# Kernel tuning notes

Hardware: AMD Instinct MI355X
Metric: run time of the kernel (lower is better)

The kernel has to match this reference:

```python
import jax, jax.numpy as jnp
import numpy as np

DIM = 768
H = 12          # num query heads
KV = 6          # num kv heads
GS = H // KV    # group size = 2
HD = DIM // H   # head dim = 64


def setup_inputs() -> dict:
    key = jax.random.key(0)
    ks = jax.random.split(key, 6)
    B, P = 8, 1024
    s = DIM ** -0.5
    x = jax.random.normal(ks[0], (B, P, DIM), dtype=jnp.float32)
    Wq = jax.random.normal(ks[1], (DIM, DIM), dtype=jnp.float32) * s
    Wk = jax.random.normal(ks[2], (DIM, KV * HD), dtype=jnp.float32) * s
    Wv = jax.random.normal(ks[3], (DIM, KV * HD), dtype=jnp.float32) * s
    Wp = jax.random.normal(ks[4], (DIM, DIM), dtype=jnp.float32) * s
    bp = jnp.zeros((DIM,), dtype=jnp.float32)
    return {"x": x, "Wq": Wq, "Wk": Wk, "Wv": Wv, "Wp": Wp, "bp": bp}


def reference(x, Wq, Wk, Wv, Wp, bp):
    B, P, C = x.shape
    scale = HD ** -0.5
    # projections; consecutive heads i*GS..(i+1)*GS-1 form kv-group i (torch.split dim=1)
    q = (x @ Wq).reshape(B, P, KV, GS, HD).transpose(0, 2, 3, 1, 4) * scale  # [B,KV,GS,P,d]
    k = (x @ Wk).reshape(B, P, KV, HD).transpose(0, 2, 1, 3)                 # [B,KV,P,d]
    v = (x @ Wv).reshape(B, P, KV, HD).transpose(0, 2, 1, 3)                 # [B,KV,P,d]

    scores = jnp.einsum('bghqd,bgkd->bghqk', q, k)      # [B,KV,GS,P,P]
    w = jax.nn.softmax(scores, axis=-1)                  # attn_drop=0 (eval)
    att = jnp.einsum('bghqk,bgkd->bghqd', w, v)          # [B,KV,GS,P,d]

    # per-group row-matched gaussian-ish noise (torch get_gaussian), vectorized over KV groups
    y = P * HD
    flat = att.reshape(B, KV, GS, y)                     # rows = groups within kv-group
    M = jax.random.uniform(jax.random.key(42), (KV, GS, y), dtype=flat.dtype)
    di = jnp.arange(min(GS, y))
    M = M.at[:, di, di].set(0.0)                         # sparse: zero diagonal
    m_mean = M.mean(axis=-1, keepdims=True)
    m_std = jnp.std(M, axis=-1, ddof=1, keepdims=True)   # torch.std is unbiased
    m_std = jnp.where(m_std == 0, jnp.ones_like(m_std), m_std)
    Z = (M - m_mean) / m_std                             # [KV,GS,y], shared across batch
    r_mean = flat.mean(axis=-1, keepdims=True)           # [B,KV,GS,1]
    r_std = jnp.std(flat, axis=-1, ddof=1, keepdims=True)
    flat = flat - (Z[None] * r_std + r_mean)

    att = flat.reshape(B, KV, GS, P, HD).reshape(B, H, P, HD)
    out = att.transpose(0, 2, 1, 3).reshape(B, P, C) @ Wp + bp  # proj_drop=0
    return out
```

## Files before the change

### kernel.cpp

```cpp
#include <hip/hip_runtime.h>
#include <hip/hip_bf16.h>
#include <math.h>


#define NTHREADS 256

typedef __bf16 bf16x8 __attribute__((ext_vector_type(8)));
typedef float f32x4 __attribute__((ext_vector_type(4)));

#define MFMA16(a, b, c) __builtin_amdgcn_mfma_f32_16x16x32_bf16(a, b, c, 0, 0, 0)

#define QSCALE 0.18033688011112042f

__device__ __forceinline__ float fexp2(float x) {
#if __has_builtin(__builtin_amdgcn_exp2f)
    return __builtin_amdgcn_exp2f(x);
#else
    return __expf(x * 0.6931471805599453f);
#endif
}

__device__ __forceinline__ void gload16(const void* g, void* l) {
    __builtin_amdgcn_global_load_lds(
        (const __attribute__((address_space(1))) void*)g,
        (__attribute__((address_space(3))) void*)l, 16, 0, 0);
}

__device__ __forceinline__ unsigned rotl_u32(unsigned x, int r) {
    return (x << r) | (x >> (32 - r));
}
__device__ __forceinline__ void threefry_0_42(unsigned x0, unsigned x1,
                                              unsigned& o0, unsigned& o1) {
    const unsigned ks0 = 0u, ks1 = 42u, ks2 = 0u ^ 42u ^ 0x1BD11BDAu;
    x0 += ks0; x1 += ks1;
#define R4(a,b,c,d) \
    x0 += x1; x1 = rotl_u32(x1,a); x1 ^= x0; \
    x0 += x1; x1 = rotl_u32(x1,b); x1 ^= x0; \
    x0 += x1; x1 = rotl_u32(x1,c); x1 ^= x0; \
    x0 += x1; x1 = rotl_u32(x1,d); x1 ^= x0;
    R4(13,15,26,6)   x0 += ks1; x1 += ks2 + 1u;
    R4(17,29,16,24)  x0 += ks2; x1 += ks0 + 2u;
    R4(13,15,26,6)   x0 += ks0; x1 += ks1 + 3u;
    R4(17,29,16,24)  x0 += ks1; x1 += ks2 + 4u;
    R4(13,15,26,6)   x0 += ks2; x1 += ks0 + 5u;
#undef R4
    o0 = x0; o1 = x1;
}
__device__ __forceinline__ float tf_uniform(unsigned i) {
    unsigned o0, o1;
    threefry_0_42(0u, i, o0, o1);
    unsigned bits = o0 ^ o1;
    return __uint_as_float((bits >> 9) | 0x3f800000u) - 1.0f;
}

__device__ __forceinline__ float wave_sum64(float v) {
#pragma unroll
    for (int off = 32; off; off >>= 1) v += __shfl_xor(v, off, 64);
    return v;
}

__device__ __forceinline__ unsigned short bf16_rne(float x) {
    unsigned u = __float_as_uint(x);
    return (unsigned short)((u + 0x7fffu + ((u >> 16) & 1u)) >> 16);
}
__device__ __forceinline__ unsigned pack_bf16x2(float lo, float hi) {
    return (unsigned)bf16_rne(lo) | ((unsigned)bf16_rne(hi) << 16);
}
__device__ __forceinline__ float bfu(unsigned v) {
    return __uint_as_float(v << 16);
}

__global__ __launch_bounds__(NTHREADS) void prep_k(
    const float* __restrict__ x, const float* __restrict__ Wq,
    const float* __restrict__ Wk, const float* __restrict__ Wv,
    const float* __restrict__ Wp,
    unsigned short* __restrict__ xb, unsigned short* __restrict__ wqt,
    unsigned short* __restrict__ wkt, unsigned short* __restrict__ wvt,
    unsigned short* __restrict__ wpt,
    unsigned short* __restrict__ zb, float* __restrict__ zpart)
{
    __shared__ float rbuf[8];
    int blk = blockIdx.x;
    if (blk < 1536) {
#pragma unroll
        for (int j = 0; j < 4; ++j) {
            int i = blk * 1024 + j * 256 + threadIdx.x;
            float4 v = ((const float4*)x)[i];
            uint2 u;
            u.x = pack_bf16x2(v.x, v.y);
            u.y = pack_bf16x2(v.z, v.w);
            *(uint2*)(xb + (size_t)i * 4) = u;
        }
    } else if (blk < 1920) {
        int zc = blk - 1536;
        int row = zc >> 5, chunk = zc & 31;
        int g = row & 1;
        int j0 = chunk * 2048;
        float sum = 0.f, sumsq = 0.f;
        for (int t = threadIdx.x; t < 2048; t += NTHREADS) {
            int j = j0 + t;
            unsigned i = (unsigned)row * 65536u + (unsigned)j;
            float m = tf_uniform(i);
            if (j == g) m = 0.f;
            zb[i] = bf16_rne(m);
            sum += m; sumsq += m * m;
        }
        sum = wave_sum64(sum); sumsq = wave_sum64(sumsq);
        int lane = threadIdx.x & 63, wv = threadIdx.x >> 6;
        if (lane == 0) { rbuf[wv] = sum; rbuf[4 + wv] = sumsq; }
        __syncthreads();
        if (threadIdx.x == 0) {
            zpart[zc * 2]     = rbuf[0] + rbuf[1] + rbuf[2] + rbuf[3];
            zpart[zc * 2 + 1] = rbuf[4] + rbuf[5] + rbuf[6] + rbuf[7];
        }
    } else {
        int id = blk - 1920;
        const float* W; unsigned short* Wt; int N;
        if (id < 144)      { W = Wq; Wt = wqt; N = 768; }
        else if (id < 216) { W = Wk; Wt = wkt; N = 384; id -= 144; }
        else if (id < 288) { W = Wv; Wt = wvt; N = 384; id -= 216; }
        else               { W = Wp; Wt = wpt; N = 768; id -= 288; }
        int ntn = N >> 6;
        int kt = id / ntn, nt = id % ntn;
        int k0 = kt * 64, n0 = nt * 64;
        int t = threadIdx.x;
        int tn = t & 63, tk = t >> 6;
        float r[16];
#pragma unroll
        for (int j = 0; j < 16; ++j)
            r[j] = W[(size_t)(k0 + tk * 16 + j) * N + n0 + tn];
        uint4 u0, u1;
        u0.x = pack_bf16x2(r[0], r[1]);   u0.y = pack_bf16x2(r[2], r[3]);
        u0.z = pack_bf16x2(r[4], r[5]);   u0.w = pack_bf16x2(r[6], r[7]);
        u1.x = pack_bf16x2(r[8], r[9]);   u1.y = pack_bf16x2(r[10], r[11]);
        u1.z = pack_bf16x2(r[12], r[13]); u1.w = pack_bf16x2(r[14], r[15]);
        unsigned short* dst = Wt + (size_t)(n0 + tn) * 768 + k0 + tk * 16;
        *(uint4*)dst = u0;
        *(uint4*)(dst + 8) = u1;
    }
}

__device__ __forceinline__ void mfma_tile_compute(
    const unsigned short* __restrict__ A, const unsigned short* __restrict__ Bt,
    int row0, int col0,
    unsigned short* As, unsigned short* Bs, f32x4 acc[4][4])
{
    const int tid = threadIdx.x;
    const int w = tid >> 6, lane = tid & 63;
    const int c = lane & 15, g = lane >> 4;
    const int m0 = (w & 1) * 64, n0 = (w >> 1) * 64;

#pragma unroll
    for (int mi = 0; mi < 4; ++mi)
#pragma unroll
        for (int ni = 0; ni < 4; ++ni) acc[mi][ni] = (f32x4){0.f, 0.f, 0.f, 0.f};

    const unsigned short* Ag0 = A + (size_t)(row0 + w * 16 + c) * 768 + g * 8;
    const unsigned short* Ag1 = A + (size_t)(row0 + (w + 4) * 16 + c) * 768 + g * 8;
    const unsigned short* Bg0 = Bt + (size_t)(col0 + w * 16 + c) * 768 + g * 8;
    const unsigned short* Bg1 = Bt + (size_t)(col0 + (w + 4) * 16 + c) * 768 + g * 8;
    unsigned short* Al0 = As + w * 1024 + lane * 8;
    unsigned short* Al1 = As + (w + 4) * 1024 + lane * 8;
    unsigned short* Bl0 = Bs + w * 1024 + lane * 8;
    unsigned short* Bl1 = Bs + (w + 4) * 1024 + lane * 8;

    for (int k0 = 0; k0 < 768; k0 += 64) {
        __syncthreads();
        gload16(Ag0 + k0,      Al0);
        gload16(Ag0 + k0 + 32, Al0 + 512);
        gload16(Ag1 + k0,      Al1);
        gload16(Ag1 + k0 + 32, Al1 + 512);
        gload16(Bg0 + k0,      Bl0);
        gload16(Bg0 + k0 + 32, Bl0 + 512);
        gload16(Bg1 + k0,      Bl1);
        gload16(Bg1 + k0 + 32, Bl1 + 512);
        __syncthreads();
#pragma unroll
        for (int ks = 0; ks < 2; ++ks) {
            bf16x8 aA[4], bB[4];
#pragma unroll
            for (int mi = 0; mi < 4; ++mi)
                aA[mi] = *(const bf16x8*)&As[(size_t)((m0 >> 4) + mi) * 1024 + ks * 512 + g * 128 + c * 8];
#pragma unroll
            for (int ni = 0; ni < 4; ++ni)
                bB[ni] = *(const bf16x8*)&Bs[(size_t)((n0 >> 4) + ni) * 1024 + ks * 512 + g * 128 + c * 8];
#pragma unroll
            for (int mi = 0; mi < 4; ++mi)
#pragma unroll
                for (int ni = 0; ni < 4; ++ni)
                    acc[mi][ni] = MFMA16(aA[mi], bB[ni], acc[mi][ni]);
        }
    }
}

__global__ __launch_bounds__(NTHREADS) void qkv_mfma_k(
    const unsigned short* __restrict__ xb, const unsigned short* __restrict__ wqt,
    const unsigned short* __restrict__ wkt, const unsigned short* __restrict__ wvt,
    unsigned short* __restrict__ qbh, unsigned short* __restrict__ kb2,
    unsigned short* __restrict__ vb2)
{
    __shared__ unsigned short As[8192];
    __shared__ unsigned short Bs[8192];
    int nb = blockIdx.x;
    int y0 = blockIdx.y * 128;
    f32x4 acc[4][4];

    const int tid = threadIdx.x;
    const int w = tid >> 6, lane = tid & 63;
    const int c = lane & 15, g = lane >> 4;
    const int m0 = (w & 1) * 64, n0 = (w >> 1) * 64;

    if (nb < 9) {
        int row0 = (nb < 6) ? nb * 128 : (nb - 6) * 128;
        const unsigned short* Wt = (nb < 6) ? wqt : wkt;
        mfma_tile_compute(Wt, xb, row0, y0, As, Bs, acc);
        float scale = (nb < 6) ? QSCALE : 1.0f;
#pragma unroll
        for (int mi = 0; mi < 4; ++mi) {
            int ocol = row0 + m0 + mi * 16 + g * 4;
#pragma unroll
            for (int ni = 0; ni < 4; ++ni) {
                int pglob = y0 + n0 + ni * 16 + c;
                int b = pglob >> 10, pin = pglob & 1023;
                ushort4 u;
                u.x = bf16_rne(acc[mi][ni][0] * scale);
                u.y = bf16_rne(acc[mi][ni][1] * scale);
                u.z = bf16_rne(acc[mi][ni][2] * scale);
                u.w = bf16_rne(acc[mi][ni][3] * scale);
                if (nb < 6) {
                    int h = ocol >> 6, d0 = ocol & 63;
                    *(ushort4*)&qbh[(((size_t)b * 12 + h) * 1024 + pin) * 64 + d0] = u;
                } else {
                    int kv = ocol >> 6, d0 = ocol & 63;
                    int kt = pin >> 7, key = pin & 127;
                    *(ushort4*)&kb2[((((size_t)(b * 6 + kv) * 8 + kt) * 8 + (d0 >> 3)) * 128
                                     + key) * 8 + (d0 & 7)] = u;
                }
            }
        }
    } else {
        int col0 = (nb - 9) * 128;
        mfma_tile_compute(xb, wvt, y0, col0, As, Bs, acc);
#pragma unroll
        for (int mi = 0; mi < 4; ++mi) {
            int pglob = y0 + m0 + mi * 16 + g * 4;
            int b = pglob >> 10, pin = pglob & 1023;
            int kt = pin >> 7, pg = (pin & 127) >> 3, p8 = pin & 7;
#pragma unroll
            for (int ni = 0; ni < 4; ++ni) {
                int vcol = col0 + n0 + ni * 16 + c;
                int kv = vcol >> 6, d = vcol & 63;
                ushort4 u;
                u.x = bf16_rne(acc[mi][ni][0]);
                u.y = bf16_rne(acc[mi][ni][1]);
                u.z = bf16_rne(acc[mi][ni][2]);
                u.w = bf16_rne(acc[mi][ni][3]);
                *(ushort4*)&vb2[((((size_t)(b * 6 + kv) * 8 + kt) * 16 + pg) * 64 + d) * 8 + p8] = u;
            }
        }
    }
}

__global__ __launch_bounds__(NTHREADS) void proj_mfma_k(
    const unsigned short* __restrict__ attb, const unsigned short* __restrict__ wpt,
    const float* __restrict__ bp, float* __restrict__ out)
{
    __shared__ unsigned short As[8192];
    __shared__ unsigned short Bs[8192];
    int row0 = blockIdx.x * 128, col0 = blockIdx.y * 128;
    f32x4 acc[4][4];
    mfma_tile_compute(wpt, attb, row0, col0, As, Bs, acc);

    const int tid = threadIdx.x;
    const int w = tid >> 6, lane = tid & 63;
    const int c = lane & 15, g = lane >> 4;
    const int m0 = (w & 1) * 64, n0 = (w >> 1) * 64;
#pragma unroll
    for (int mi = 0; mi < 4; ++mi) {
        int ocol = row0 + m0 + mi * 16 + g * 4;
        float4 bias = *(const float4*)&bp[ocol];
#pragma unroll
        for (int ni = 0; ni < 4; ++ni) {
            int p = col0 + n0 + ni * 16 + c;
            float4 u;
            u.x = acc[mi][ni][0] + bias.x;
            u.y = acc[mi][ni][1] + bias.y;
            u.z = acc[mi][ni][2] + bias.z;
            u.w = acc[mi][ni][3] + bias.w;
            *(float4*)&out[(size_t)p * 768 + ocol] = u;
        }
    }
}

#define LDP 136
__global__ __launch_bounds__(NTHREADS) void attn_mfma_k(
    const unsigned short* __restrict__ qbh, const unsigned short* __restrict__ kb2,
    const unsigned short* __restrict__ vb2, unsigned short* __restrict__ attb,
    float* __restrict__ spart)
{
    __shared__ unsigned short P_lds[4 * 32 * LDP];
    __shared__ float l_s[4][32];
    __shared__ float sbuf[8];

    const int qt0 = blockIdx.x * 128;
    const int h = blockIdx.y, b = blockIdx.z, kv = h >> 1;
    const int tid = threadIdx.x;
    const int w = tid >> 6, lane = tid & 63;
    const int c = lane & 15, g = lane >> 4;

    const unsigned short* qh = qbh + (((size_t)b * 12 + h) * 1024 + qt0 + w * 32) * 64;
    const unsigned short* kbase = kb2 + ((size_t)(b * 6 + kv) * 8) * 8192;
    const unsigned short* vbase = vb2 + ((size_t)(b * 6 + kv) * 8) * 8192;
    unsigned short* Pw = P_lds + w * 32 * LDP;

    bf16x8 bQ[2][2];
#pragma unroll
    for (int ks = 0; ks < 2; ++ks) {
        bQ[ks][0] = *(const bf16x8*)(qh + (size_t)(c) * 64 + ks * 32 + g * 8);
        bQ[ks][1] = *(const bf16x8*)(qh + (size_t)(16 + c) * 64 + ks * 32 + g * 8);
    }

    f32x4 O[2][4];
#pragma unroll
    for (int i = 0; i < 2; ++i)
#pragma unroll
        for (int j = 0; j < 4; ++j) O[i][j] = (f32x4){0.f, 0.f, 0.f, 0.f};
    float l_r[2] = {0.f, 0.f};

    for (int t = 0; t < 8; ++t) {
        const unsigned short* kt = kbase + (size_t)t * 8192;
        const unsigned short* vt = vbase + (size_t)t * 8192;

        bf16x8 aK[2][8];
#pragma unroll
        for (int ks = 0; ks < 2; ++ks)
#pragma unroll
            for (int mb = 0; mb < 8; ++mb)
                aK[ks][mb] = *(const bf16x8*)(kt + ((size_t)(ks * 4 + g) * 128 + mb * 16 + c) * 8);

        f32x4 S[8][2];
#pragma unroll
        for (int mb = 0; mb < 8; ++mb) {
            S[mb][0] = (f32x4){0.f, 0.f, 0.f, 0.f};
            S[mb][1] = (f32x4){0.f, 0.f, 0.f, 0.f};
        }
#pragma unroll
        for (int ks = 0; ks < 2; ++ks)
#pragma unroll
            for (int mb = 0; mb < 8; ++mb) {
                S[mb][0] = MFMA16(aK[ks][mb], bQ[ks][0], S[mb][0]);
                S[mb][1] = MFMA16(aK[ks][mb], bQ[ks][1], S[mb][1]);
            }

        bf16x8 bV[4][4];
#pragma unroll
        for (int ks = 0; ks < 4; ++ks)
#pragma unroll
            for (int nb = 0; nb < 4; ++nb)
                bV[ks][nb] = *(const bf16x8*)(vt + ((size_t)(ks * 4 + g) * 64 + nb * 16 + c) * 8);

#pragma unroll
        for (int qn = 0; qn < 2; ++qn) {
            float lt = 0.f;
#pragma unroll
            for (int mb = 0; mb < 8; ++mb) {
                float p0 = fexp2(S[mb][qn][0]);
                float p1 = fexp2(S[mb][qn][1]);
                float p2 = fexp2(S[mb][qn][2]);
                float p3 = fexp2(S[mb][qn][3]);
                lt += (p0 + p1) + (p2 + p3);
                uint2 uu;
                uu.x = pack_bf16x2(p0, p1);
                uu.y = pack_bf16x2(p2, p3);
                *(uint2*)&Pw[(size_t)(qn * 16 + c) * LDP + mb * 16 + g * 4] = uu;
            }
            lt += __shfl_xor(lt, 16, 64);
            lt += __shfl_xor(lt, 32, 64);
            l_r[qn] += lt;
        }

#pragma unroll
        for (int ks = 0; ks < 4; ++ks) {
            bf16x8 aP0 = *(const bf16x8*)&Pw[(size_t)(c) * LDP + ks * 32 + g * 8];
            bf16x8 aP1 = *(const bf16x8*)&Pw[(size_t)(16 + c) * LDP + ks * 32 + g * 8];
#pragma unroll
            for (int nb = 0; nb < 4; ++nb) {
                O[0][nb] = MFMA16(aP0, bV[ks][nb], O[0][nb]);
                O[1][nb] = MFMA16(aP1, bV[ks][nb], O[1][nb]);
            }
        }
    }
    if (g == 0) { l_s[w][c] = l_r[0]; l_s[w][16 + c] = l_r[1]; }
    f32x4 li0 = *(f32x4*)&l_s[w][g * 4];
    f32x4 li1 = *(f32x4*)&l_s[w][16 + g * 4];
    float inv0[4], inv1[4];
#pragma unroll
    for (int r = 0; r < 4; ++r) { inv0[r] = 1.f / li0[r]; inv1[r] = 1.f / li1[r]; }
    unsigned short* ob = attb + ((size_t)b * 1024 + qt0 + w * 32) * 768 + h * 64;
    float psum = 0.f, psumsq = 0.f;
#pragma unroll
    for (int r = 0; r < 4; ++r) {
#pragma unroll
        for (int nb = 0; nb < 4; ++nb) {
            float o0 = O[0][nb][r] * inv0[r];
            float o1 = O[1][nb][r] * inv1[r];
            psum += o0 + o1;
            psumsq += o0 * o0 + o1 * o1;
            ob[(size_t)(g * 4 + r) * 768 + nb * 16 + c]      = bf16_rne(o0);
            ob[(size_t)(16 + g * 4 + r) * 768 + nb * 16 + c] = bf16_rne(o1);
        }
    }
    psum = wave_sum64(psum); psumsq = wave_sum64(psumsq);
    if (lane == 0) { sbuf[w] = psum; sbuf[4 + w] = psumsq; }
    __syncthreads();
    if (tid == 0) {
        int idx = ((b * 12 + h) * 8 + blockIdx.x) * 2;
        spart[idx]     = sbuf[0] + sbuf[1] + sbuf[2] + sbuf[3];
        spart[idx + 1] = sbuf[4] + sbuf[5] + sbuf[6] + sbuf[7];
    }
}

__global__ __launch_bounds__(NTHREADS) void stats2_k(
    unsigned short* __restrict__ attb, const unsigned short* __restrict__ zb,
    const float* __restrict__ spart, const float* __restrict__ zpart)
{
    int blk = blockIdx.x;
    int bh = blk >> 3, ch = blk & 7;
    int b = bh / 12, h = bh % 12;
    float zs = 0.f, zs2 = 0.f, rs = 0.f, rs2 = 0.f;
#pragma unroll
    for (int cc = 0; cc < 32; ++cc) {
        zs  += zpart[(h * 32 + cc) * 2];
        zs2 += zpart[(h * 32 + cc) * 2 + 1];
    }
#pragma unroll
    for (int cc = 0; cc < 8; ++cc) {
        rs  += spart[(bh * 8 + cc) * 2];
        rs2 += spart[(bh * 8 + cc) * 2 + 1];
    }
    float m_mean = zs * (1.f / 65536.f);
    float m_var  = (zs2 - 65536.f * m_mean * m_mean) * (1.f / 65535.f);
    float m_sd   = sqrtf(fmaxf(m_var, 0.f));
    if (m_sd == 0.f) m_sd = 1.f;
    float r_mean = rs * (1.f / 65536.f);
    float r_var  = (rs2 - 65536.f * r_mean * r_mean) * (1.f / 65535.f);
    float r_sd   = sqrtf(fmaxf(r_var, 0.f));
    float a = r_sd / m_sd;
    float bc = m_mean * a - r_mean;

    unsigned short* base = attb + ((size_t)b * 1024 + ch * 128) * 768 + h * 64;
    const unsigned short* zrow = zb + (size_t)h * 65536 + (size_t)ch * 8192;
    for (int f = threadIdx.x; f < 1024; f += NTHREADS) {
        int p = f >> 3, dq = (f & 7) * 8;
        unsigned short* ptr = base + (size_t)p * 768 + dq;
        uint4 u = *(const uint4*)ptr;
        uint4 zu = *(const uint4*)(zrow + (size_t)f * 8);
        float v0 = bfu(u.x)       - bfu(zu.x)       * a + bc;
        float v1 = bfu(u.x >> 16) - bfu(zu.x >> 16) * a + bc;
        float v2 = bfu(u.y)       - bfu(zu.y)       * a + bc;
        float v3 = bfu(u.y >> 16) - bfu(zu.y >> 16) * a + bc;
        float v4 = bfu(u.z)       - bfu(zu.z)       * a + bc;
        float v5 = bfu(u.z >> 16) - bfu(zu.z >> 16) * a + bc;
        float v6 = bfu(u.w)       - bfu(zu.w)       * a + bc;
        float v7 = bfu(u.w >> 16) - bfu(zu.w >> 16) * a + bc;
        uint4 o;
        o.x = pack_bf16x2(v0, v1);
        o.y = pack_bf16x2(v2, v3);
        o.z = pack_bf16x2(v4, v5);
        o.w = pack_bf16x2(v6, v7);
        *(uint4*)ptr = o;
    }
}

extern "C" void kernel_launch(void* const* d_in, const int* in_sizes, int n_in,
                              void* d_out, int out_size, void* d_ws, size_t ws_size,
                              hipStream_t stream) {
    const float* x  = (const float*)d_in[0];
    const float* Wq = (const float*)d_in[1];
    const float* Wk = (const float*)d_in[2];
    const float* Wv = (const float*)d_in[3];
    const float* Wp = (const float*)d_in[4];
    const float* bp = (const float*)d_in[5];
    float* out = (float*)d_out;

    float* ws    = (float*)d_ws;
    float* zpart = ws;
    float* spart = zpart + 768;
    unsigned short* zb   = (unsigned short*)(spart + 1536);
    unsigned short* xb   = zb + 786432;
    unsigned short* wqt  = xb + 6291456;
    unsigned short* wkt  = wqt + 589824;
    unsigned short* wvt  = wkt + 294912;
    unsigned short* wpt  = wvt + 294912;
    unsigned short* qbh  = wpt + 589824;
    unsigned short* kb2  = qbh + 6291456;
    unsigned short* vb2  = kb2 + 3145728;
    unsigned short* attb = vb2 + 3145728;

    prep_k<<<2352, NTHREADS, 0, stream>>>(x, Wq, Wk, Wv, Wp,
                                          xb, wqt, wkt, wvt, wpt, zb, zpart);
    qkv_mfma_k<<<dim3(12, 64), NTHREADS, 0, stream>>>(xb, wqt, wkt, wvt, qbh, kb2, vb2);
    attn_mfma_k<<<dim3(8, 12, 8), NTHREADS, 0, stream>>>(qbh, kb2, vb2, attb, spart);
    stats2_k<<<768, NTHREADS, 0, stream>>>(attb, zb, spart, zpart);
    proj_mfma_k<<<dim3(6, 64), NTHREADS, 0, stream>>>(attb, wpt, bp, out);
}
```

Before: 222.4 us.

## Double-buffer LDS tiles in MFMA GEMM to overlap global loads with compute

Splits the shared tile buffers into two sets and restructures the K loop so the next 64-wide K slice is fetched into one buffer while MFMAs run on the other. This halves the barriers per slice and hides global-to-LDS latency behind compute in the QKV and output projection GEMMs. LDS use per block doubles to 64 KB, which may cut occupancy. The gload-to-LDS completion still depends on the barrier for correctness.

```diff
diff --git a/kernel.cpp b/kernel.cpp
--- a/kernel.cpp
+++ b/kernel.cpp
@@ -143,7 +143,9 @@
 __device__ __forceinline__ void mfma_tile_compute(
     const unsigned short* __restrict__ A, const unsigned short* __restrict__ Bt,
     int row0, int col0,
-    unsigned short* As, unsigned short* Bs, f32x4 acc[4][4])
+    unsigned short* As0, unsigned short* Bs0,
+    unsigned short* As1, unsigned short* Bs1,
+    f32x4 acc[4][4])
 {
     const int tid = threadIdx.x;
     const int w = tid >> 6, lane = tid & 63;
@@ -159,38 +161,57 @@
     const unsigned short* Ag1 = A + (size_t)(row0 + (w + 4) * 16 + c) * 768 + g * 8;
     const unsigned short* Bg0 = Bt + (size_t)(col0 + w * 16 + c) * 768 + g * 8;
     const unsigned short* Bg1 = Bt + (size_t)(col0 + (w + 4) * 16 + c) * 768 + g * 8;
-    unsigned short* Al0 = As + w * 1024 + lane * 8;
-    unsigned short* Al1 = As + (w + 4) * 1024 + lane * 8;
-    unsigned short* Bl0 = Bs + w * 1024 + lane * 8;
-    unsigned short* Bl1 = Bs + (w + 4) * 1024 + lane * 8;
-
-    for (int k0 = 0; k0 < 768; k0 += 64) {
+    const int l0 = w * 1024 + lane * 8;
+    const int l1 = (w + 4) * 1024 + lane * 8;
+
+#define STAGE_TILE(k0, As, Bs) do {                                           \
+        gload16(Ag0 + (k0),      (As) + l0);                                  \
+        gload16(Ag0 + (k0) + 32, (As) + l0 + 512);                            \
+        gload16(Ag1 + (k0),      (As) + l1);                                  \
+        gload16(Ag1 + (k0) + 32, (As) + l1 + 512);                            \
+        gload16(Bg0 + (k0),      (Bs) + l0);                                  \
+        gload16(Bg0 + (k0) + 32, (Bs) + l0 + 512);                            \
+        gload16(Bg1 + (k0),      (Bs) + l1);                                  \
+        gload16(Bg1 + (k0) + 32, (Bs) + l1 + 512);                            \
+    } while (0)
+
+#define COMPUTE_TILE(As, Bs) do {                                             \
+        _Pragma("unroll")                                                     \
+        for (int ks = 0; ks < 2; ++ks) {                                      \
+            bf16x8 aA[4], bB[4];                                              \
+            _Pragma("unroll")                                                 \
+            for (int mi = 0; mi < 4; ++mi)                                    \
+                aA[mi] = *(const bf16x8*)&(As)[(size_t)((m0 >> 4) + mi) * 1024\
+                                               + ks * 512 + g * 128 + c * 8]; \
+            _Pragma("unroll")                                                 \
+            for (int ni = 0; ni < 4; ++ni)                                    \
+                bB[ni] = *(const bf16x8*)&(Bs)[(size_t)((n0 >> 4) + ni) * 1024\
+                                               + ks * 512 + g * 128 + c * 8]; \
+            _Pragma("unroll")                                                 \
+            for (int mi = 0; mi < 4; ++mi)                                    \
+                _Pragma("unroll")                                             \
+                for (int ni = 0; ni < 4; ++ni)                                \
+                    acc[mi][ni] = MFMA16(aA[mi], bB[ni], acc[mi][ni]);        \
+        }                                                                     \
+    } while (0)
+
+    STAGE_TILE(0, As0, Bs0);
+    __syncthreads();
+    for (int k0 = 64; k0 <= 576; k0 += 128) {
+        STAGE_TILE(k0, As1, Bs1);
+        COMPUTE_TILE(As0, Bs0);
         __syncthreads();
-        gload16(Ag0 + k0,      Al0);
-        gload16(Ag0 + k0 + 32, Al0 + 512);
-        gload16(Ag1 + k0,      Al1);
-        gload16(Ag1 + k0 + 32, Al1 + 512);
-        gload16(Bg0 + k0,      Bl0);
-        gload16(Bg0 + k0 + 32, Bl0 + 512);
-        gload16(Bg1 + k0,      Bl1);
-        gload16(Bg1 + k0 + 32, Bl1 + 512);
+        STAGE_TILE(k0 + 64, As0, Bs0);
+        COMPUTE_TILE(As1, Bs1);
         __syncthreads();
-#pragma unroll
-        for (int ks = 0; ks < 2; ++ks) {
-            bf16x8 aA[4], bB[4];
-#pragma unroll
-            for (int mi = 0; mi < 4; ++mi)
-                aA[mi] = *(const bf16x8*)&As[(size_t)((m0 >> 4) + mi) * 1024 + ks * 512 + g * 128 + c * 8];
-#pragma unroll
-            for (int ni = 0; ni < 4; ++ni)
-                bB[ni] = *(const bf16x8*)&Bs[(size_t)((n0 >> 4) + ni) * 1024 + ks * 512 + g * 128 + c * 8];
-#pragma unroll
-            for (int mi = 0; mi < 4; ++mi)
-#pragma unroll
-                for (int ni = 0; ni < 4; ++ni)
-                    acc[mi][ni] = MFMA16(aA[mi], bB[ni], acc[mi][ni]);
-        }
-    }
+    }
+    STAGE_TILE(704, As1, Bs1);
+    COMPUTE_TILE(As0, Bs0);
+    __syncthreads();
+    COMPUTE_TILE(As1, Bs1);
+
+#undef STAGE_TILE
+#undef COMPUTE_TILE
 }
 
 __global__ __launch_bounds__(NTHREADS) void qkv_mfma_k(
@@ -199,8 +220,7 @@
     unsigned short* __restrict__ qbh, unsigned short* __restrict__ kb2,
     unsigned short* __restrict__ vb2)
 {
-    __shared__ unsigned short As[8192];
-    __shared__ unsigned short Bs[8192];
+    __shared__ unsigned short As0[8192], Bs0[8192], As1[8192], Bs1[8192];
     int nb = blockIdx.x;
     int y0 = blockIdx.y * 128;
     f32x4 acc[4][4];
@@ -213,7 +233,7 @@
     if (nb < 9) {
         int row0 = (nb < 6) ? nb * 128 : (nb - 6) * 128;
         const unsigned short* Wt = (nb < 6) ? wqt : wkt;
-        mfma_tile_compute(Wt, xb, row0, y0, As, Bs, acc);
+        mfma_tile_compute(Wt, xb, row0, y0, As0, Bs0, As1, Bs1, acc);
         float scale = (nb < 6) ? QSCALE : 1.0f;
 #pragma unroll
         for (int mi = 0; mi < 4; ++mi) {
@@ -240,7 +260,7 @@
         }
     } else {
         int col0 = (nb - 9) * 128;
-        mfma_tile_compute(xb, wvt, y0, col0, As, Bs, acc);
+        mfma_tile_compute(xb, wvt, y0, col0, As0, Bs0, As1, Bs1, acc);
 #pragma unroll
         for (int mi = 0; mi < 4; ++mi) {
             int pglob = y0 + m0 + mi * 16 + g * 4;
@@ -265,11 +285,10 @@
     const unsigned short* __restrict__ attb, const unsigned short* __restrict__ wpt,
     const float* __restrict__ bp, float* __restrict__ out)
 {
-    __shared__ unsigned short As[8192];
-    __shared__ unsigned short Bs[8192];
+    __shared__ unsigned short As0[8192], Bs0[8192], As1[8192], Bs1[8192];
     int row0 = blockIdx.x * 128, col0 = blockIdx.y * 128;
     f32x4 acc[4][4];
-    mfma_tile_compute(wpt, attb, row0, col0, As, Bs, acc);
+    mfma_tile_compute(wpt, attb, row0, col0, As0, Bs0, As1, Bs1, acc);
 
     const int tid = threadIdx.x;
     const int w = tid >> 6, lane = tid & 63;
```

Result: no change. 224.3 us (+0.8%).
